# Kernel optimization log

Hardware: AMD Instinct MI355X
Metric: run time of the kernel (lower is better)

Reference implementation:

```python
import jax, jax.numpy as jnp
import numpy as np
from itertools import product

C_IN, C_OUT = 32, 64
N_DOWN = 100000
CHILD = 4
N = N_DOWN * CHILD  # 400000 active voxels


def _encode(c):
    # pack nonnegative (x,y,z) voxel coords into a single int64 key
    c = c.astype(np.int64)
    return (c[:, 0] << 40) | (c[:, 1] << 20) | c[:, 2]


def _build_coords(rng):
    # N_DOWN unique parent voxels in [1,126]^3, each with exactly CHILD distinct children
    flat = rng.choice(126 ** 3, N_DOWN, replace=False)
    px = flat // (126 * 126) + 1
    py = (flat // 126) % 126 + 1
    pz = flat % 126 + 1
    parents = np.stack([px, py, pz], 1)  # [N_DOWN,3]
    child_off = rng.random((N_DOWN, 8)).argsort(1)[:, :CHILD]  # [N_DOWN,4] in 0..7
    bits = np.stack([child_off >> 2 & 1, child_off >> 1 & 1, child_off & 1], -1)  # [N_DOWN,4,3]
    children = (2 * parents[:, None, :] + bits).reshape(N, 3)
    kvec = child_off.reshape(N)  # kernel offset id of each child within its parent
    parent_of = np.repeat(np.arange(N_DOWN), CHILD)
    return children, kvec, parent_of


def _build_kmap3(children):
    # submanifold 3x3x3 neighbor map: km_in[k,i] = index j with coords[j] = coords[i] + off_k
    keys = _encode(children)
    order = np.argsort(keys)
    skeys = keys[order]
    offsets = list(product((-1, 0, 1), repeat=3))
    km_in = np.full((27, N), N, np.int32)
    km_out = np.full((27, N), N, np.int32)
    ar = np.arange(N, dtype=np.int32)
    for k, off in enumerate(offsets):
        nk = _encode(children + np.asarray(off))
        pos = np.clip(np.searchsorted(skeys, nk), 0, N - 1)
        found = skeys[pos] == nk
        km_in[k] = np.where(found, order[pos].astype(np.int32), N)
        km_out[k] = np.where(found, ar, N)
    return km_in, km_out


def _build_kmap_pool(kvec, parent_of):
    # kernel-2 stride-2 conv: each child feeds exactly one parent at offset kvec
    kp_in = np.full((8, N), N, np.int32)
    kp_out = np.full((8, N), N_DOWN, np.int32)
    for k in range(8):
        idx = np.nonzero(kvec == k)[0]
        kp_in[k, :len(idx)] = idx
        kp_out[k, :len(idx)] = parent_of[idx]
    return kp_in, kp_out


def setup_inputs() -> dict:
    rng = np.random.default_rng(0)
    children, kvec, parent_of = _build_coords(rng)
    km_in, km_out = _build_kmap3(children)
    kp_in, kp_out = _build_kmap_pool(kvec, parent_of)

    key = jax.random.key(0)
    ks = jax.random.split(key, 10)
    f32 = jnp.float32
    return {
        'x': jax.random.normal(ks[0], (N, C_IN), f32),
        'W1': jax.random.normal(ks[1], (27, C_IN, C_OUT), f32) * 0.05,
        'bn1_s': jax.random.uniform(ks[2], (C_OUT,), f32, 0.5, 1.5),
        'bn1_b': jax.random.normal(ks[3], (C_OUT,), f32) * 0.1,
        'W2': jax.random.normal(ks[4], (27, C_OUT, C_OUT), f32) * 0.05,
        'bn2_s': jax.random.uniform(ks[5], (C_OUT,), f32, 0.5, 1.5),
        'bn2_b': jax.random.normal(ks[6], (C_OUT,), f32) * 0.1,
        'Wp': jax.random.normal(ks[7], (8, C_OUT, C_OUT), f32) * 0.05,
        'bnp_s': jax.random.uniform(ks[8], (C_OUT,), f32, 0.5, 1.5),
        'bnp_b': jax.random.normal(ks[9], (C_OUT,), f32) * 0.1,
        'km_in': jnp.asarray(km_in),
        'km_out': jnp.asarray(km_out),
        'kp_in': jnp.asarray(kp_in),
        'kp_out': jnp.asarray(kp_out),
        'n_down': N_DOWN,
    }


def _sparse_conv(x, W, iidx, oidx, n_out):
    # gather -> per-offset matmul -> scatter-add; invalid pairs point at zero row / dump row
    xp = jnp.concatenate([x, jnp.zeros((1, x.shape[1]), x.dtype)], 0)
    def body(acc, a):
        Wk, ii, oi = a
        return acc.at[oi].add(xp[ii] @ Wk), None
    acc0 = jnp.zeros((n_out + 1, W.shape[2]), x.dtype)
    acc, _ = jax.lax.scan(body, acc0, (W, iidx, oidx))
    return acc[:n_out]


def _bn_relu(h, s, b):
    return jax.nn.relu(h * s + b)


def reference(x, W1, bn1_s, bn1_b, W2, bn2_s, bn2_b, Wp, bnp_s, bnp_b,
              km_in, km_out, kp_in, kp_out, n_down):
    n = x.shape[0]
    h = _bn_relu(_sparse_conv(x, W1, km_in, km_out, n), bn1_s, bn1_b)
    down = _bn_relu(_sparse_conv(h, W2, km_in, km_out, n), bn2_s, bn2_b)
    p = _bn_relu(_sparse_conv(down, Wp, kp_in, kp_out, n_down), bnp_s, bnp_b)
    return (down, p)
```

## Files before the change

### kernel.cpp

```cpp
#include <hip/hip_runtime.h>


#define NV 400000
#define ND 100000

typedef __attribute__((ext_vector_type(8))) short  bf16x8;
typedef __attribute__((ext_vector_type(4))) float  f32x4;

__device__ __forceinline__ unsigned short f2b(float f) {
    unsigned int u = __builtin_bit_cast(unsigned int, f);
    u += 0x7fffu + ((u >> 16) & 1u);
    return (unsigned short)(u >> 16);
}

__global__ __launch_bounds__(256) void cvt_bf16_k(
    const float* __restrict__ in, unsigned short* __restrict__ out, int n)
{
    int t = (blockIdx.x * 256 + threadIdx.x) * 4;
    if (t >= n) return;
    float4 f = *(const float4*)(in + t);
    ushort4 u;
    u.x = f2b(f.x); u.y = f2b(f.y); u.z = f2b(f.z); u.w = f2b(f.w);
    *(ushort4*)(out + t) = u;
}

__global__ __launch_bounds__(256) void pack_w_k(
    const float* __restrict__ W, unsigned short* __restrict__ out, int nk, int ci)
{
    int t = blockIdx.x * 256 + threadIdx.x;
    int steps = ci >> 5;
    if (t >= nk * steps * 4 * 64) return;
    int lane = t & 63;
    int nt   = (t >> 6) & 3;
    int rest = t >> 8;
    int s    = rest % steps;
    int k    = rest / steps;
    int col = lane & 15, quad = lane >> 4;
    int co = nt * 16 + col;
    unsigned short v[8];
#pragma unroll
    for (int j = 0; j < 8; ++j) {
        int cidx = s * 32 + quad * 8 + j;
        v[j] = f2b(W[((size_t)k * ci + cidx) * 64 + co]);
    }
    bf16x8 frag;
#pragma unroll
    for (int j = 0; j < 8; ++j) frag[j] = (short)v[j];
    *(bf16x8*)(out + (size_t)t * 8) = frag;
}

__global__ __launch_bounds__(256) void ck_init_k(int* __restrict__ ck)
{
    int t = blockIdx.x * 256 + threadIdx.x;
    if (t < ND * 8) ck[t] = NV;
}
__global__ __launch_bounds__(256) void ck_scatter_k(
    const int* __restrict__ kp_in, const int* __restrict__ kp_out,
    int* __restrict__ ck)
{
    int t = blockIdx.x * 256 + threadIdx.x;
    if (t >= 8 * NV) return;
    int j = kp_in[t];
    if (j == NV) return;
    int k = t / NV;
    ck[(size_t)k * ND + kp_out[t]] = j;
}

template <int CI, int G>
__device__ __forceinline__ void conv_group(
    const unsigned short* __restrict__ xin,
    const unsigned short* __restrict__ Wp,
    const int* __restrict__ km, int nr, int kg,
    const int rowm[4], int lane, int quad,
    f32x4 acc[4][4])
{
    constexpr int STEPS = CI / 32;
    int j[G][4];
#pragma unroll
    for (int g = 0; g < G; ++g)
#pragma unroll
        for (int mt = 0; mt < 4; ++mt)
            j[g][mt] = km[(size_t)(kg + g) * nr + rowm[mt]];

#pragma unroll
    for (int s = 0; s < STEPS; ++s) {
        bf16x8 a[G][4];
#pragma unroll
        for (int g = 0; g < G; ++g)
#pragma unroll
            for (int mt = 0; mt < 4; ++mt)
                a[g][mt] = *(const bf16x8*)(
                    xin + (size_t)j[g][mt] * CI + s * 32 + quad * 8);
#pragma unroll
        for (int g = 0; g < G; ++g) {
            const unsigned short* bp =
                Wp + ((((size_t)(kg + g) * STEPS + s) * 4) * 64 + lane) * 8;
#pragma unroll
            for (int nt = 0; nt < 4; ++nt) {
                bf16x8 b = *(const bf16x8*)(bp + (size_t)nt * 512);
#pragma unroll
                for (int mt = 0; mt < 4; ++mt)
                    acc[mt][nt] = __builtin_amdgcn_mfma_f32_16x16x32_bf16(
                        a[g][mt], b, acc[mt][nt], 0, 0, 0);
            }
        }
    }
}

template <int CI, int NK, int MODE, int NR>
__global__ __launch_bounds__(256, 3) void conv_mfma(
    const unsigned short* __restrict__ xin,
    const unsigned short* __restrict__ Wp,
    const int* __restrict__ km,
    const float* __restrict__ bns, const float* __restrict__ bnb,
    float* __restrict__ outf, unsigned short* __restrict__ outb)
{
    constexpr int G = (CI == 32) ? 4 : 3;
    const int lane = threadIdx.x & 63;
    const int wave = threadIdx.x >> 6;
    const int col = lane & 15, quad = lane >> 4;
    const int wbase = (blockIdx.x * 4 + wave) * 64;

    int rowm[4];
#pragma unroll
    for (int mt = 0; mt < 4; ++mt) {
        int r = wbase + mt * 16 + col;
        rowm[mt] = r < NR ? r : NR - 1;
    }

    f32x4 acc[4][4];
#pragma unroll
    for (int mt = 0; mt < 4; ++mt)
#pragma unroll
        for (int nt = 0; nt < 4; ++nt) acc[mt][nt] = (f32x4)0.f;

    constexpr int NFULL = (NK / G) * G;
    for (int kg = 0; kg < NFULL; kg += G)
        conv_group<CI, G>(xin, Wp, km, NR, kg, rowm, lane, quad, acc);
    if constexpr (NK % G != 0)
        conv_group<CI, NK % G>(xin, Wp, km, NR, NFULL, rowm, lane, quad, acc);

#pragma unroll
    for (int nt = 0; nt < 4; ++nt) {
        const int n = nt * 16 + col;
        const float sc = bns[n], bi = bnb[n];
#pragma unroll
        for (int mt = 0; mt < 4; ++mt)
#pragma unroll
            for (int r = 0; r < 4; ++r) {
                int row = wbase + mt * 16 + quad * 4 + r;
                if (row < NR) {
                    float v = fmaxf(fmaf(acc[mt][nt][r], sc, bi), 0.f);
                    if constexpr (MODE == 0) {
                        outf[(size_t)row * 64 + n] = v;
                    } else if constexpr (MODE == 1) {
                        outb[(size_t)row * 64 + n] = f2b(v);
                    } else {
                        outf[(size_t)row * 64 + n] = v;
                        outb[(size_t)row * 64 + n] = f2b(v);
                    }
                }
            }
    }
}

extern "C" void kernel_launch(void* const* d_in, const int* in_sizes, int n_in,
                              void* d_out, int out_size, void* d_ws, size_t ws_size,
                              hipStream_t stream)
{
    const float* x    = (const float*)d_in[0];
    const float* W1   = (const float*)d_in[1];
    const float* bn1s = (const float*)d_in[2];
    const float* bn1b = (const float*)d_in[3];
    const float* W2   = (const float*)d_in[4];
    const float* bn2s = (const float*)d_in[5];
    const float* bn2b = (const float*)d_in[6];
    const float* Wp   = (const float*)d_in[7];
    const float* bnps = (const float*)d_in[8];
    const float* bnpb = (const float*)d_in[9];
    const int* km_in  = (const int*)d_in[10];
    const int* kp_in  = (const int*)d_in[12];
    const int* kp_out = (const int*)d_in[13];

    float* down = (float*)d_out;
    float* pout = (float*)d_out + (size_t)NV * 64;

    char* ws = (char*)d_ws;
    unsigned short* x_bf  = (unsigned short*)ws;  ws += (size_t)(NV + 1) * 32 * 2;
    unsigned short* h_bf  = (unsigned short*)ws;  ws += (size_t)(NV + 1) * 64 * 2;
    unsigned short* d_bf  = (unsigned short*)ws;  ws += (size_t)(NV + 1) * 64 * 2;
    int*            ck    = (int*)ws;             ws += (size_t)8 * ND * 4;
    unsigned short* W1p   = (unsigned short*)ws;  ws += (size_t)27 * 32 * 64 * 2;
    unsigned short* W2p   = (unsigned short*)ws;  ws += (size_t)27 * 64 * 64 * 2;
    unsigned short* Wpp   = (unsigned short*)ws;

    hipMemsetAsync(x_bf + (size_t)NV * 32, 0, 32 * 2, stream);
    hipMemsetAsync(h_bf + (size_t)NV * 64, 0, 64 * 2, stream);
    hipMemsetAsync(d_bf + (size_t)NV * 64, 0, 64 * 2, stream);

    cvt_bf16_k<<<(NV * 32 / 4 + 255) / 256, 256, 0, stream>>>(x, x_bf, NV * 32);
    pack_w_k<<<(27 * 1 * 4 * 64 + 255) / 256, 256, 0, stream>>>(W1, W1p, 27, 32);
    pack_w_k<<<(27 * 2 * 4 * 64 + 255) / 256, 256, 0, stream>>>(W2, W2p, 27, 64);
    pack_w_k<<<(8  * 2 * 4 * 64 + 255) / 256, 256, 0, stream>>>(Wp, Wpp, 8, 64);
    ck_init_k<<<(ND * 8 + 255) / 256, 256, 0, stream>>>(ck);
    ck_scatter_k<<<(8 * NV + 255) / 256, 256, 0, stream>>>(kp_in, kp_out, ck);

    const int cgrid = (NV + 255) / 256;
    conv_mfma<32, 27, 1, NV><<<cgrid, 256, 0, stream>>>(
        x_bf, W1p, km_in, bn1s, bn1b, nullptr, h_bf);
    conv_mfma<64, 27, 2, NV><<<cgrid, 256, 0, stream>>>(
        h_bf, W2p, km_in, bn2s, bn2b, down, d_bf);
    conv_mfma<64, 8, 0, ND><<<(ND + 255) / 256, 256, 0, stream>>>(
        d_bf, Wpp, ck, bnps, bnpb, pout, nullptr);
}
```

Baseline: 620.4 us.

## Halve rows per wave, drop offset grouping, remap blocks across XCDs

Each wave now covers 32 output rows instead of 64, and the loop walks one kernel offset at a time instead of batching 3-4 offsets of gathers. This shrinks accumulator and gather registers so the launch bound can rise from 3 to 4 blocks per CU, giving more waves to hide gather latency. Block IDs are remapped so consecutive row ranges sit on the same XCD, which should improve L2 locality of neighbouring gathers. The cost is less memory-level parallelism per wave, since fewer gathers are in flight before each MFMA, and each weight fragment is reused across fewer rows.

```diff
diff --git a/kernel.cpp b/kernel.cpp
--- a/kernel.cpp
+++ b/kernel.cpp
@@ -66,91 +66,73 @@
     ck[(size_t)k * ND + kp_out[t]] = j;
 }
 
-template <int CI, int G>
-__device__ __forceinline__ void conv_group(
-    const unsigned short* __restrict__ xin,
-    const unsigned short* __restrict__ Wp,
-    const int* __restrict__ km, int nr, int kg,
-    const int rowm[4], int lane, int quad,
-    f32x4 acc[4][4])
-{
-    constexpr int STEPS = CI / 32;
-    int j[G][4];
-#pragma unroll
-    for (int g = 0; g < G; ++g)
-#pragma unroll
-        for (int mt = 0; mt < 4; ++mt)
-            j[g][mt] = km[(size_t)(kg + g) * nr + rowm[mt]];
-
-#pragma unroll
-    for (int s = 0; s < STEPS; ++s) {
-        bf16x8 a[G][4];
-#pragma unroll
-        for (int g = 0; g < G; ++g)
-#pragma unroll
-            for (int mt = 0; mt < 4; ++mt)
-                a[g][mt] = *(const bf16x8*)(
-                    xin + (size_t)j[g][mt] * CI + s * 32 + quad * 8);
-#pragma unroll
-        for (int g = 0; g < G; ++g) {
-            const unsigned short* bp =
-                Wp + ((((size_t)(kg + g) * STEPS + s) * 4) * 64 + lane) * 8;
-#pragma unroll
-            for (int nt = 0; nt < 4; ++nt) {
-                bf16x8 b = *(const bf16x8*)(bp + (size_t)nt * 512);
-#pragma unroll
-                for (int mt = 0; mt < 4; ++mt)
-                    acc[mt][nt] = __builtin_amdgcn_mfma_f32_16x16x32_bf16(
-                        a[g][mt], b, acc[mt][nt], 0, 0, 0);
-            }
-        }
-    }
-}
-
 template <int CI, int NK, int MODE, int NR>
-__global__ __launch_bounds__(256, 3) void conv_mfma(
+__global__ __launch_bounds__(256, 4) void conv_mfma(
     const unsigned short* __restrict__ xin,
     const unsigned short* __restrict__ Wp,
     const int* __restrict__ km,
     const float* __restrict__ bns, const float* __restrict__ bnb,
     float* __restrict__ outf, unsigned short* __restrict__ outb)
 {
-    constexpr int G = (CI == 32) ? 4 : 3;
+    constexpr int STEPS = CI / 32;
     const int lane = threadIdx.x & 63;
     const int wave = threadIdx.x >> 6;
     const int col = lane & 15, quad = lane >> 4;
-    const int wbase = (blockIdx.x * 4 + wave) * 64;
 
-    int rowm[4];
+    const int nwg = gridDim.x;
+    const int q = nwg >> 3, r = nwg & 7;
+    const int xcd = blockIdx.x & 7, bodd = blockIdx.x >> 3;
+    const int bid = (xcd < r ? xcd * (q + 1) : r * (q + 1) + (xcd - r) * q) + bodd;
+
+    const int wbase = (bid * 4 + wave) * 32;
+
+    int rowm[2];
 #pragma unroll
-    for (int mt = 0; mt < 4; ++mt) {
-        int r = wbase + mt * 16 + col;
-        rowm[mt] = r < NR ? r : NR - 1;
+    for (int mt = 0; mt < 2; ++mt) {
+        int rr = wbase + mt * 16 + col;
+        rowm[mt] = rr < NR ? rr : NR - 1;
     }
 
-    f32x4 acc[4][4];
+    f32x4 acc[2][4];
 #pragma unroll
-    for (int mt = 0; mt < 4; ++mt)
+    for (int mt = 0; mt < 2; ++mt)
 #pragma unroll
         for (int nt = 0; nt < 4; ++nt) acc[mt][nt] = (f32x4)0.f;
 
-    constexpr int NFULL = (NK / G) * G;
-    for (int kg = 0; kg < NFULL; kg += G)
-        conv_group<CI, G>(xin, Wp, km, NR, kg, rowm, lane, quad, acc);
-    if constexpr (NK % G != 0)
-        conv_group<CI, NK % G>(xin, Wp, km, NR, NFULL, rowm, lane, quad, acc);
+    for (int k = 0; k < NK; ++k) {
+        const int* __restrict__ kmr = km + (size_t)k * NR;
+        int j[2];
+#pragma unroll
+        for (int mt = 0; mt < 2; ++mt) j[mt] = kmr[rowm[mt]];
+#pragma unroll
+        for (int s = 0; s < STEPS; ++s) {
+            bf16x8 a[2];
+#pragma unroll
+            for (int mt = 0; mt < 2; ++mt)
+                a[mt] = *(const bf16x8*)(xin + (size_t)j[mt] * CI + s * 32 + quad * 8);
+            const unsigned short* bp = Wp + ((((size_t)k * STEPS + s) * 4) * 64 + lane) * 8;
+#pragma unroll
+            for (int nt = 0; nt < 4; ++nt) {
+                bf16x8 b = *(const bf16x8*)(bp + (size_t)nt * 512);
+#pragma unroll
+                for (int mt = 0; mt < 2; ++mt)
+                    acc[mt][nt] = __builtin_amdgcn_mfma_f32_16x16x32_bf16(
+                        a[mt], b, acc[mt][nt], 0, 0, 0);
+            }
+        }
+    }
 
 #pragma unroll
     for (int nt = 0; nt < 4; ++nt) {
         const int n = nt * 16 + col;
         const float sc = bns[n], bi = bnb[n];
 #pragma unroll
-        for (int mt = 0; mt < 4; ++mt)
+        for (int mt = 0; mt < 2; ++mt)
 #pragma unroll
-            for (int r = 0; r < 4; ++r) {
-                int row = wbase + mt * 16 + quad * 4 + r;
+            for (int rr = 0; rr < 4; ++rr) {
+                int row = wbase + mt * 16 + quad * 4 + rr;
                 if (row < NR) {
-                    float v = fmaxf(fmaf(acc[mt][nt][r], sc, bi), 0.f);
+                    float v = fmaxf(fmaf(acc[mt][nt][rr], sc, bi), 0.f);
                     if constexpr (MODE == 0) {
                         outf[(size_t)row * 64 + n] = v;
                     } else if constexpr (MODE == 1) {
@@ -205,11 +187,11 @@
     ck_init_k<<<(ND * 8 + 255) / 256, 256, 0, stream>>>(ck);
     ck_scatter_k<<<(8 * NV + 255) / 256, 256, 0, stream>>>(kp_in, kp_out, ck);
 
-    const int cgrid = (NV + 255) / 256;
+    const int cgrid = (NV + 127) / 128;
     conv_mfma<32, 27, 1, NV><<<cgrid, 256, 0, stream>>>(
         x_bf, W1p, km_in, bn1s, bn1b, nullptr, h_bf);
     conv_mfma<64, 27, 2, NV><<<cgrid, 256, 0, stream>>>(
         h_bf, W2p, km_in, bn2s, bn2b, down, d_bf);
-    conv_mfma<64, 8, 0, ND><<<(ND + 255) / 256, 256, 0, stream>>>(
+    conv_mfma<64, 8, 0, ND><<<(ND + 127) / 128, 256, 0, stream>>>(
         d_bf, Wpp, ck, bnps, bnpb, pout, nullptr);
 }
```

Result: no change. 629.0 us (+1.4%).
